# Performance work log

Measured on AMD Instinct MI355X. Metric: run time of the kernel, lower is better.

The kernel has to match this reference:

```python
import jax, jax.numpy as jnp
import numpy as np

B, S, D, P, NQ = 8, 2048, 1024, 256, 8192


def setup_inputs() -> dict:
    key = jax.random.key(0)
    ks = jax.random.split(key, 8)
    return {
        "flag": 0,
        "encoded_input": jax.random.normal(ks[0], (B, S, D), dtype=jnp.float32),
        "start_ids_1": jax.random.randint(ks[1], (NQ,), 0, S, dtype=jnp.int32),
        "end_ids_1": jax.random.randint(ks[2], (NQ,), 0, S, dtype=jnp.int32),
        "query_batch_idx": jax.random.randint(ks[3], (NQ,), 0, B, dtype=jnp.int32),
        "start_ids_2": jax.random.randint(ks[4], (NQ,), 0, S, dtype=jnp.int32),
        "end_ids_2": jax.random.randint(ks[5], (NQ,), 0, S, dtype=jnp.int32),
        "W": jax.random.normal(ks[6], (D, P), dtype=jnp.float32) * 0.02,
        "b": jnp.zeros((P,), dtype=jnp.float32),
    }


def _gather_spans(h, qb, s, e):
    # span_repr[b, i, j] = concat(h[b, i], h[b, j]) for j >= i, else 0.
    # Direct gather instead of building the O(seq^2) table.
    rep = jnp.concatenate([h[qb, s], h[qb, e]], axis=-1)  # [NQ, 2*P]
    valid = (e >= s).astype(rep.dtype)[:, None]
    return rep * valid


def reference(flag, encoded_input, start_ids_1, end_ids_1, query_batch_idx,
              start_ids_2, end_ids_2, W, b):
    h = encoded_input @ W + b  # [B, S, P] (use_proj=True)
    res1 = _gather_spans(h, query_batch_idx, start_ids_1, end_ids_1)
    res2 = _gather_spans(h, query_batch_idx, start_ids_2, end_ids_2)
    return (res1, res2)
```

## Files before the change

kernel.cpp:

```cpp
#include <hip/hip_runtime.h>
#include <hip/hip_bf16.h>
#include <stdint.h>

#define S_LEN 2048
#define D_DIM 1024
#define P_DIM 256
#define NQ_   8192
#define M_TOT 16384
#define CAP 32
#define HS  260

typedef __attribute__((ext_vector_type(4))) float  f32x4;
typedef __attribute__((ext_vector_type(8))) __bf16 bf16x8;


__global__ __launch_bounds__(1024) void wtf_kernel(const float* __restrict__ W,
                                                   __bf16* __restrict__ WTf,
                                                   int* __restrict__ cnt) {
    __shared__ float tile[32][33];
    const int bx = blockIdx.x;
    const int by = blockIdx.y;
    const int k0 = bx * 32, n0 = by * 32;
    const int tx = threadIdx.x, ty = threadIdx.y;
    const int g = (by * 32 + bx) * 1024 + ty * 32 + tx;
    if (g < M_TOT) cnt[g] = 0;
    tile[ty][tx] = W[(k0 + ty) * P_DIM + (n0 + tx)];
    __syncthreads();
    const int t = ty * 32 + tx;
    if (t < 128) {
        const int c16r = t >> 6, q = (t >> 4) & 3, lm = t & 15;
        bf16x8 v;
        #pragma unroll
        for (int e = 0; e < 8; ++e) v[e] = (__bf16)tile[q * 8 + e][c16r * 16 + lm];
        const int c16 = by * 2 + c16r;
        const int ts  = bx >> 1, kh = bx & 1;
        *(bf16x8*)(WTf + (size_t)((c16 * 32 + ts * 2 + kh) * 512 + (q * 16 + lm) * 8)) = v;
    }
}

__global__ __launch_bounds__(256) void index_zero(const int* __restrict__ s1,
                                                  const int* __restrict__ e1,
                                                  const int* __restrict__ s2,
                                                  const int* __restrict__ e2,
                                                  const int* __restrict__ qb,
                                                  int* __restrict__ cnt,
                                                  int* __restrict__ bucket,
                                                  float* __restrict__ out) {
    const int lane = threadIdx.x & 63;
    const int q    = blockIdx.x * 64 + lane;
    const int set  = threadIdx.x >> 7;
    const int half = (threadIdx.x >> 6) & 1;
    const int b    = qb[q];
    const int s = set ? s2[q] : s1[q];
    const int e = set ? e2[q] : e1[q];
    if (!half && e >= s) {
        int r = b * S_LEN + s;
        int k = atomicAdd(&cnt[r], 1); if (k < CAP) bucket[r * CAP + k] = (q << 2) | (set << 1);
        r = b * S_LEN + e;
        k = atomicAdd(&cnt[r], 1);     if (k < CAP) bucket[r * CAP + k] = (q << 2) | (set << 1) | 1;
    }
    unsigned long long mask = __ballot(e < s);
    const int bqw = blockIdx.x * 64;
    const float4 z = make_float4(0.f, 0.f, 0.f, 0.f);
    while (mask) {
        const int j = __ffsll(mask) - 1;
        mask &= mask - 1;
        float* dst = out + (size_t)set * (NQ_ * 512) + (size_t)(bqw + j) * 512 + half * 256;
        ((float4*)dst)[lane] = z;
    }
}

__global__ __launch_bounds__(512, 1) void gemm_kernel(const float*  __restrict__ A,
                                                      const __bf16* __restrict__ WTf,
                                                      const float*  __restrict__ bias,
                                                      const int*    __restrict__ cnt,
                                                      const int*    __restrict__ bucket,
                                                      float*        __restrict__ out) {
    __shared__ __align__(16) __bf16 Afl[65536];
    __shared__ int s_cnt[64];
    __shared__ int s_off[65];
    __shared__ int elist[64 * CAP];

    const int tid = threadIdx.x;
    const int w   = tid >> 6;
    const int l   = tid & 63;
    const int lm  = l & 15;
    const int q   = l >> 4;

    const int m0 = blockIdx.x * 64;
    const int ph = (blockIdx.x * 5) & 15;

    const __bf16* bp[2][2];
    #pragma unroll
    for (int ni = 0; ni < 2; ++ni)
        #pragma unroll
        for (int kh = 0; kh < 2; ++kh)
            bp[ni][kh] = WTf + (size_t)(((w * 2 + ni) * 32 + kh) * 512 + l * 8);

    bf16x8 bre[3][2][2];
#define LOADB(B, T) {                                                         \
    const int kt_ = ((T) + ph) & 15;                                          \
    _Pragma("unroll") for (int ni = 0; ni < 2; ++ni)                          \
        _Pragma("unroll") for (int kh = 0; kh < 2; ++kh)                      \
            bre[B][ni][kh] = *(const bf16x8*)(bp[ni][kh] + kt_ * 1024); }

    LOADB(0, 0)
    LOADB(1, 1)

    {
        const int r   = tid >> 3;
        const int la  = tid & 7;
        const int mi  = r >> 4, lmr = r & 15;
        const float* src = A + (size_t)(m0 + r) * D_DIM;
        #pragma unroll
        for (int it = 0; it < 16; ++it) {
            const int c = it * 8 + la;
            const float4 x0 = *(const float4*)(src + c * 8);
            const float4 x1 = *(const float4*)(src + c * 8 + 4);
            bf16x8 v;
            v[0] = (__bf16)x0.x; v[1] = (__bf16)x0.y; v[2] = (__bf16)x0.z; v[3] = (__bf16)x0.w;
            v[4] = (__bf16)x1.x; v[5] = (__bf16)x1.y; v[6] = (__bf16)x1.z; v[7] = (__bf16)x1.w;
            const int kt = c >> 3, kh = (c >> 2) & 1, qp = c & 3;
            const int slot = lmr ^ (qp << 1);
            *(bf16x8*)(&Afl[(mi * 32 + kt * 2 + kh) * 512 + qp * 128 + slot * 8]) = v;
        }
    }
    __syncthreads();

    const int slotr = lm ^ (q << 1);
    const __bf16* abase = Afl + q * 128 + slotr * 8;
    f32x4 acc[4][2] = {};

    #pragma unroll
    for (int t = 0; t < 16; ++t) {
        if (t < 14) LOADB((t + 2) % 3, t + 2)
        const int kt_ = (t + ph) & 15;
        bf16x8 af[4][2];
        #pragma unroll
        for (int mi = 0; mi < 4; ++mi)
            #pragma unroll
            for (int kh = 0; kh < 2; ++kh)
                af[mi][kh] = *(const bf16x8*)(abase + (mi * 32 + kt_ * 2 + kh) * 512);
        #pragma unroll
        for (int kh = 0; kh < 2; ++kh)
            #pragma unroll
            for (int mi = 0; mi < 4; ++mi)
                #pragma unroll
                for (int ni = 0; ni < 2; ++ni)
                    acc[mi][ni] = __builtin_amdgcn_mfma_f32_16x16x32_bf16(
                        af[mi][kh], bre[t % 3][ni][kh], acc[mi][ni], 0, 0, 0);
    }
#undef LOADB

    __syncthreads();
    float* hs = (float*)Afl;

    if (tid < 64) { int c = cnt[m0 + tid]; s_cnt[tid] = c < CAP ? c : CAP; }

    #pragma unroll
    for (int ni = 0; ni < 2; ++ni) {
        const int col = w * 32 + ni * 16 + lm;
        const float bv = bias[col];
        #pragma unroll
        for (int mi = 0; mi < 4; ++mi) {
            const int rbase = mi * 16 + q * 4;
            #pragma unroll
            for (int r = 0; r < 4; ++r)
                hs[(rbase + r) * HS + col] = acc[mi][ni][r] + bv;
        }
    }
    __syncthreads();
    if (tid == 0) {
        int a = 0;
        #pragma unroll 1
        for (int i = 0; i < 64; ++i) { s_off[i] = a; a += s_cnt[i]; }
        s_off[64] = a;
    }
    __syncthreads();
    if (tid < 64) {
        const int o = s_off[tid], c = s_cnt[tid];
        const int* bk = bucket + (size_t)(m0 + tid) * CAP;
        for (int k = 0; k < c; ++k)
            elist[o + k] = (tid << 15) | (bk[k] & 0x7fff);
    }
    __syncthreads();

    const int E   = s_off[64];
    const int grp = tid >> 6;
    const int gl  = tid & 63;
    #pragma unroll 1
    for (int j = grp; j < E; j += 8) {
        const int ent  = elist[j];
        const int rl   = ent >> 15;
        const int code = ent & 0x7fff;
        const int qq   = code >> 2;
        const int st   = (code >> 1) & 1;
        const int hf   = code & 1;
        const float4 v = *(const float4*)&hs[rl * HS + gl * 4];
        *(float4*)(out + (size_t)st * (NQ_ * 512) + (size_t)qq * 512 + hf * 256 + gl * 4) = v;
    }
}

extern "C" void kernel_launch(void* const* d_in, const int* in_sizes, int n_in,
                              void* d_out, int out_size, void* d_ws, size_t ws_size,
                              hipStream_t stream) {
    const float* A    = (const float*)d_in[1];
    const int*   s1   = (const int*)  d_in[2];
    const int*   e1   = (const int*)  d_in[3];
    const int*   qb   = (const int*)  d_in[4];
    const int*   s2   = (const int*)  d_in[5];
    const int*   e2   = (const int*)  d_in[6];
    const float* W    = (const float*)d_in[7];
    const float* bias = (const float*)d_in[8];
    float*       out  = (float*)d_out;

    __bf16* WTf    = (__bf16*)d_ws;
    int*    cnt    = (int*)((char*)d_ws + (1 << 20));
    int*    bucket = (int*)((char*)d_ws + (1 << 20) + (1 << 16));

    wtf_kernel <<<dim3(32, 8), dim3(32, 32), 0, stream>>>(W, WTf, cnt);
    index_zero <<<dim3(NQ_ / 64), dim3(256), 0, stream>>>(s1, e1, s2, e2, qb, cnt, bucket, out);
    gemm_kernel<<<dim3(M_TOT / 64), dim3(512), 0, stream>>>(A, WTf, bias, cnt, bucket, out);
}
```

Baseline: 133.9 us.

## Pipeline A-tile global loads and bf16 conversion with MFMA compute in quarters

The GEMM kernel previously loaded and converted the entire 64x1024 A tile into LDS before starting any MFMA work. It now splits K into four quarters: each quarter is loaded from global memory into registers one stage ahead, converted and written to LDS, then computed while the next quarter loads. The per-block K phase rotation is coarsened from 16 steps to 4 quarter offsets so that compute order matches the order quarters arrive. This aims to hide global load latency behind compute, at the cost of more register pressure (16 float4 buffers) and extra barriers.

```diff
diff --git a/kernel.cpp b/kernel.cpp
--- a/kernel.cpp
+++ b/kernel.cpp
@@ -87,8 +87,8 @@
     const int lm  = l & 15;
     const int q   = l >> 4;
 
-    const int m0 = blockIdx.x * 64;
-    const int ph = (blockIdx.x * 5) & 15;
+    const int m0  = blockIdx.x * 64;
+    const int ph4 = blockIdx.x & 3;
 
     const __bf16* bp[2][2];
     #pragma unroll
@@ -98,8 +98,9 @@
             bp[ni][kh] = WTf + (size_t)(((w * 2 + ni) * 32 + kh) * 512 + l * 8);
 
     bf16x8 bre[3][2][2];
+#define KT_OF(T) ((((ph4 + ((T) >> 2)) & 3) << 2) + ((T) & 3))
 #define LOADB(B, T) {                                                         \
-    const int kt_ = ((T) + ph) & 15;                                          \
+    const int kt_ = KT_OF(T);                                                 \
     _Pragma("unroll") for (int ni = 0; ni < 2; ++ni)                          \
         _Pragma("unroll") for (int kh = 0; kh < 2; ++kh)                      \
             bre[B][ni][kh] = *(const bf16x8*)(bp[ni][kh] + kt_ * 1024); }
@@ -107,50 +108,69 @@
     LOADB(0, 0)
     LOADB(1, 1)
 
-    {
-        const int r   = tid >> 3;
-        const int la  = tid & 7;
-        const int mi  = r >> 4, lmr = r & 15;
-        const float* src = A + (size_t)(m0 + r) * D_DIM;
-        #pragma unroll
-        for (int it = 0; it < 16; ++it) {
-            const int c = it * 8 + la;
-            const float4 x0 = *(const float4*)(src + c * 8);
-            const float4 x1 = *(const float4*)(src + c * 8 + 4);
-            bf16x8 v;
-            v[0] = (__bf16)x0.x; v[1] = (__bf16)x0.y; v[2] = (__bf16)x0.z; v[3] = (__bf16)x0.w;
-            v[4] = (__bf16)x1.x; v[5] = (__bf16)x1.y; v[6] = (__bf16)x1.z; v[7] = (__bf16)x1.w;
-            const int kt = c >> 3, kh = (c >> 2) & 1, qp = c & 3;
-            const int slot = lmr ^ (qp << 1);
-            *(bf16x8*)(&Afl[(mi * 32 + kt * 2 + kh) * 512 + qp * 128 + slot * 8]) = v;
-        }
-    }
-    __syncthreads();
+    const int r    = tid >> 3;
+    const int la   = tid & 7;
+    const int mi_s = r >> 4, lmr = r & 15;
+    const float* asrc = A + (size_t)(m0 + r) * D_DIM;
+
+    float4 fA[8], fB[8];
+#define LOADQ(QQ, FR) {                                                       \
+    _Pragma("unroll") for (int it = 0; it < 4; ++it) {                        \
+        const int c = (QQ) * 32 + it * 8 + la;                                \
+        FR[it * 2]     = *(const float4*)(asrc + c * 8);                      \
+        FR[it * 2 + 1] = *(const float4*)(asrc + c * 8 + 4); } }
+#define WRITEQ(QQ, FR) {                                                      \
+    _Pragma("unroll") for (int it = 0; it < 4; ++it) {                        \
+        const int c = (QQ) * 32 + it * 8 + la;                                \
+        bf16x8 v;                                                             \
+        v[0] = (__bf16)FR[it*2].x;   v[1] = (__bf16)FR[it*2].y;               \
+        v[2] = (__bf16)FR[it*2].z;   v[3] = (__bf16)FR[it*2].w;               \
+        v[4] = (__bf16)FR[it*2+1].x; v[5] = (__bf16)FR[it*2+1].y;             \
+        v[6] = (__bf16)FR[it*2+1].z; v[7] = (__bf16)FR[it*2+1].w;             \
+        const int kt = c >> 3, kh = (c >> 2) & 1, qp = c & 3;                 \
+        const int slot = lmr ^ (qp << 1);                                     \
+        *(bf16x8*)(&Afl[(mi_s * 32 + kt * 2 + kh) * 512 + qp * 128 + slot * 8]) = v; } }
 
     const int slotr = lm ^ (q << 1);
     const __bf16* abase = Afl + q * 128 + slotr * 8;
     f32x4 acc[4][2] = {};
 
-    #pragma unroll
-    for (int t = 0; t < 16; ++t) {
-        if (t < 14) LOADB((t + 2) % 3, t + 2)
-        const int kt_ = (t + ph) & 15;
-        bf16x8 af[4][2];
-        #pragma unroll
-        for (int mi = 0; mi < 4; ++mi)
-            #pragma unroll
-            for (int kh = 0; kh < 2; ++kh)
-                af[mi][kh] = *(const bf16x8*)(abase + (mi * 32 + kt_ * 2 + kh) * 512);
-        #pragma unroll
-        for (int kh = 0; kh < 2; ++kh)
-            #pragma unroll
-            for (int mi = 0; mi < 4; ++mi)
-                #pragma unroll
-                for (int ni = 0; ni < 2; ++ni)
-                    acc[mi][ni] = __builtin_amdgcn_mfma_f32_16x16x32_bf16(
-                        af[mi][kh], bre[t % 3][ni][kh], acc[mi][ni], 0, 0, 0);
-    }
+#define CSTEP(T) {                                                            \
+    const int kt_ = KT_OF(T);                                                 \
+    bf16x8 af[4][2];                                                          \
+    _Pragma("unroll") for (int mi = 0; mi < 4; ++mi)                          \
+        _Pragma("unroll") for (int kh = 0; kh < 2; ++kh)                      \
+            af[mi][kh] = *(const bf16x8*)(abase + (mi * 32 + kt_ * 2 + kh) * 512); \
+    _Pragma("unroll") for (int kh = 0; kh < 2; ++kh)                          \
+        _Pragma("unroll") for (int mi = 0; mi < 4; ++mi)                      \
+            _Pragma("unroll") for (int ni = 0; ni < 2; ++ni)                  \
+                acc[mi][ni] = __builtin_amdgcn_mfma_f32_16x16x32_bf16(        \
+                    af[mi][kh], bre[(T) % 3][ni][kh], acc[mi][ni], 0, 0, 0); }
+
+    const int q0 = ph4, q1 = (ph4 + 1) & 3, q2 = (ph4 + 2) & 3, q3 = (ph4 + 3) & 3;
+
+    LOADQ(q0, fA)
+    LOADQ(q1, fB)
+    WRITEQ(q0, fA)
+    __syncthreads();
+    LOADB(2, 2) CSTEP(0) LOADB(0, 3) CSTEP(1) LOADB(1, 4) CSTEP(2) LOADB(2, 5) CSTEP(3)
+    WRITEQ(q1, fB)
+    LOADQ(q2, fA)
+    __syncthreads();
+    LOADB(0, 6) CSTEP(4) LOADB(1, 7) CSTEP(5) LOADB(2, 8) CSTEP(6) LOADB(0, 9) CSTEP(7)
+    WRITEQ(q2, fA)
+    LOADQ(q3, fB)
+    __syncthreads();
+    LOADB(1, 10) CSTEP(8) LOADB(2, 11) CSTEP(9) LOADB(0, 12) CSTEP(10) LOADB(1, 13) CSTEP(11)
+    WRITEQ(q3, fB)
+    __syncthreads();
+    LOADB(2, 14) CSTEP(12) LOADB(0, 15) CSTEP(13) CSTEP(14) CSTEP(15)
+
+#undef CSTEP
+#undef LOADQ
+#undef WRITEQ
 #undef LOADB
+#undef KT_OF
 
     __syncthreads();
     float* hs = (float*)Afl;
@@ -165,8 +185,8 @@
         for (int mi = 0; mi < 4; ++mi) {
             const int rbase = mi * 16 + q * 4;
             #pragma unroll
-            for (int r = 0; r < 4; ++r)
-                hs[(rbase + r) * HS + col] = acc[mi][ni][r] + bv;
+            for (int rr = 0; rr < 4; ++rr)
+                hs[(rbase + rr) * HS + col] = acc[mi][ni][rr] + bv;
         }
     }
     __syncthreads();
```

Result: no change. 132.5 us (-1.0%).
